# Kernel optimization log

Hardware: AMD Instinct MI355X
Metric: run time of the kernel (lower is better)

Reference implementation:

```python
import jax, jax.numpy as jnp
import numpy as np

B, W, K = 8, 128, 2048          # batch, window_size, n_features(=n_nodes)
D = 2 * W                        # embed_dim after the *2 in __init__ (embed_dim=None -> window_size)

def setup_inputs() -> dict:
    key = jax.random.key(0)
    k1, k2, k3, k4 = jax.random.split(key, 4)
    x = jax.random.normal(k1, (B, W, K), dtype=jnp.float32)
    # nn.Linear(2W -> D), stored as [in, out] so y = cat @ W_lin + b_lin
    lim = 1.0 / np.sqrt(2 * W)
    W_lin = jax.random.uniform(k2, (2 * W, D), dtype=jnp.float32, minval=-lim, maxval=lim)
    b_lin = jax.random.uniform(k3, (D,), dtype=jnp.float32, minval=-lim, maxval=lim)
    # a: xavier_uniform with gain=1.414 on shape (D, 1)
    a_lim = 1.414 * np.sqrt(6.0 / (D + 1))
    a = jax.random.uniform(k4, (D, 1), dtype=jnp.float32, minval=-a_lim, maxval=a_lim)
    bias = jnp.zeros((K, K), dtype=jnp.float32)
    return {"x": x, "W_lin": W_lin, "b_lin": b_lin, "a": a, "bias": bias}

def reference(x, W_lin, b_lin, a, bias):
    # x: [B, W, K] -> v: [B, K, W]
    v = jnp.transpose(x, (0, 2, 1))
    av = a[:, 0]                                  # [D]
    # lin(cat(v_i, v_j)) @ a == (v_i @ W1) @ a + (v_j @ W2) @ a + b_lin @ a
    # This avoids the O(K^2 * 2W) pairwise tensor; math identical to the original.
    W1, W2 = W_lin[:W], W_lin[W:]                 # each [W, D]
    u1 = jnp.einsum('bkw,wd,d->bk', v, W1, av)    # [B, K] source-side score
    u2 = jnp.einsum('bkw,wd,d->bk', v, W2, av)    # [B, K] target-side score
    e = u1[:, :, None] + u2[:, None, :] + jnp.dot(b_lin, av) + bias  # [B, K, K]
    attention = jax.nn.softmax(e, axis=2)         # dropout p=0.0 (eval) -> identity
    h = jax.nn.sigmoid(jnp.matmul(attention, v))  # [B, K, W]
    return jnp.transpose(h, (0, 2, 1))            # [B, W, K]
```

## Files before the change

kernel.cpp:

```cpp
#include <hip/hip_runtime.h>
#include <hip/hip_bf16.h>

#define B_ 8
#define W_ 128
#define K_ 2048
#define D_ 256
#define WX 144
#define NC 256

typedef __attribute__((ext_vector_type(8))) short bf16x8;
typedef __attribute__((ext_vector_type(4))) float f32x4;
typedef unsigned int u32;

static __device__ __forceinline__ short f2bf(float f) {
    unsigned int u = __float_as_uint(f);
    unsigned int r = (u + 0x7FFFu + ((u >> 16) & 1u)) >> 16;
    return (short)r;
}

__global__ void k_w2v(const float* __restrict__ W_lin, const float* __restrict__ a,
                      float* __restrict__ w2v) {
    int w = blockIdx.x, l = threadIdx.x;
    float4 rv = ((const float4*)(W_lin + (size_t)(W_ + w) * D_))[l];
    float4 av = ((const float4*)a)[l];
    float acc = rv.x * av.x + rv.y * av.y + rv.z * av.z + rv.w * av.w;
    for (int m = 1; m < 64; m <<= 1) acc += __shfl_xor(acc, m);
    if (l == 0) w2v[w] = acc;
}

__global__ __launch_bounds__(512) void k_pe(const float* __restrict__ x,
        const float* __restrict__ w2v, const float* __restrict__ bias,
        short* __restrict__ xbt, short* __restrict__ e2t) {
    __shared__ float sc[696];
    int tid = threadIdx.x;
    int wid = tid >> 6;
    int lane = tid & 63;

    if (blockIdx.x < 512) {
        if (tid < W_) sc[tid] = w2v[tid];
        __syncthreads();
        int q = tid & 31, cw = tid >> 5;
        int bk0 = blockIdx.x * 32;
        int b = bk0 >> 11;
        int k = (bk0 & (K_ - 1)) + q;
        const float* xp = x + ((size_t)b * W_ + cw * 8) * K_ + k;
        float xv[8];
        float acc = 0.f;
#pragma unroll
        for (int w = 0; w < 8; ++w) {
            xv[w] = xp[(size_t)w * K_];
            acc += xv[w] * sc[cw * 8 + w];
        }
        sc[128 + cw * 33 + q] = acc;
        __syncthreads();
        if (tid < 32) {
            float s = 0.f;
#pragma unroll
            for (int cc = 0; cc < 16; ++cc) s += sc[128 + cc * 33 + tid];
            sc[656 + tid] = __expf(s);
        }
        __syncthreads();
        float e1q = sc[656 + q];
        short* xo = xbt + (((size_t)b * NC + (k >> 3)) * WX + cw * 8) * 8 + (k & 7);
#pragma unroll
        for (int w = 0; w < 8; ++w) xo[w * 8] = f2bf(xv[w] * e1q);
        if (tid < 32) {
            int kk = (bk0 & (K_ - 1)) + tid;
            xbt[(((size_t)b * NC + (kk >> 3)) * WX + 128) * 8 + (kk & 7)] = f2bf(sc[656 + tid]);
        }
        if (tid >= 64 && tid < 124) {
            int id = tid - 64;
            int cl = id / 15, wz = 129 + id % 15;
            int c = ((bk0 & (K_ - 1)) >> 3) + cl;
            bf16x8 z = {0, 0, 0, 0, 0, 0, 0, 0};
            *(bf16x8*)(xbt + (((size_t)b * NC + c) * WX + wz) * 8) = z;
        }
    } else {
        int i0e = (int)(blockIdx.x - 512) * 4;
        int il = tid & 3, cg = tid >> 2;
        const float4* brow = (const float4*)(bias + (size_t)(i0e + il) * K_);
        float4 v0 = brow[cg * 4 + 0];
        float4 v1 = brow[cg * 4 + 1];
        float4 v2 = brow[cg * 4 + 2];
        float4 v3 = brow[cg * 4 + 3];
        float m = fmaxf(fmaxf(fmaxf(v0.x, v0.y), fmaxf(v0.z, v0.w)),
                        fmaxf(fmaxf(v1.x, v1.y), fmaxf(v1.z, v1.w)));
        m = fmaxf(m, fmaxf(fmaxf(fmaxf(v2.x, v2.y), fmaxf(v2.z, v2.w)),
                           fmaxf(fmaxf(v3.x, v3.y), fmaxf(v3.z, v3.w))));
#pragma unroll
        for (int mm = 4; mm < 64; mm <<= 1) m = fmaxf(m, __shfl_xor(m, mm));
        if (lane < 4) sc[wid * 4 + lane] = m;
        __syncthreads();
        float mb = sc[il];
#pragma unroll
        for (int w = 1; w < 8; ++w) mb = fmaxf(mb, sc[w * 4 + il]);
        bf16x8 o0, o1;
        o0[0] = f2bf(__expf(v0.x - mb)); o0[1] = f2bf(__expf(v0.y - mb));
        o0[2] = f2bf(__expf(v0.z - mb)); o0[3] = f2bf(__expf(v0.w - mb));
        o0[4] = f2bf(__expf(v1.x - mb)); o0[5] = f2bf(__expf(v1.y - mb));
        o0[6] = f2bf(__expf(v1.z - mb)); o0[7] = f2bf(__expf(v1.w - mb));
        o1[0] = f2bf(__expf(v2.x - mb)); o1[1] = f2bf(__expf(v2.y - mb));
        o1[2] = f2bf(__expf(v2.z - mb)); o1[3] = f2bf(__expf(v2.w - mb));
        o1[4] = f2bf(__expf(v3.x - mb)); o1[5] = f2bf(__expf(v3.y - mb));
        o1[6] = f2bf(__expf(v3.z - mb)); o1[7] = f2bf(__expf(v3.w - mb));
        int i = i0e + il;
        *(bf16x8*)(e2t + ((size_t)(cg * 2) * K_ + i) * 8)     = o0;
        *(bf16x8*)(e2t + ((size_t)(cg * 2 + 1) * K_ + i) * 8) = o1;
    }
}

#define MF(a_, b_, c_) __builtin_amdgcn_mfma_f32_16x16x32_bf16(a_, b_, c_, 0, 0, 0)

#define GLLDS(gsrc, ldst) __builtin_amdgcn_global_load_lds(                      \
    (const u32 __attribute__((address_space(1)))*)(const void*)(gsrc),           \
    (u32 __attribute__((address_space(3)))*)(void*)(ldst), 16, 0, 0)

#define WAITV(n_) asm volatile("s_waitcnt vmcnt(" #n_ ")" ::: "memory")
#define BARR __builtin_amdgcn_s_barrier()

__global__ __launch_bounds__(1024, 4) void k_gemm(const short* __restrict__ e2t,
        const short* __restrict__ xbt, float* __restrict__ out) {
    __shared__ __align__(16) char Bb[147456];
    int blk  = blockIdx.x;
    int b    = blk & 7;
    int i0   = (blk >> 3) * 64;
    int tid  = threadIdx.x;
    int wid  = tid >> 6;
    int lane = tid & 63;
    int il   = lane & 15;
    int kg   = lane >> 4;
    int m    = wid & 3;
    int jq   = wid >> 2;

    int i0r = i0 + m * 16;
    const short* eA = e2t + (((size_t)(jq * 64 + kg)) * K_ + i0r + il) * 8;
    size_t xbase = ((size_t)b * NC + jq * 64 + kg) * WX + il;
    char* jbuf = Bb + jq * 36864;

#define STG(s_) do {                                                             \
    const short* _g = xbt + (xbase + (size_t)(s_) * 4 * WX) * 8;                 \
    char* _d = jbuf + ((s_) & 3) * 9216;                                         \
    for (int f = m; f < 9; f += 4)                                               \
        GLLDS(_g + f * 128, _d + f * 1024);                                      \
} while (0)

#define FAix(sl_, s_) Ar##sl_ = *(const bf16x8*)(eA + (size_t)(s_) * 4 * K_ * 8)

    f32x4 q0{0,0,0,0}, q1{0,0,0,0}, q2{0,0,0,0}, q3{0,0,0,0}, q4{0,0,0,0},
          q5{0,0,0,0}, q6{0,0,0,0}, q7{0,0,0,0}, q8{0,0,0,0};

#define CONS(s_, sl_) do {                                                       \
    const char* _bp = jbuf + ((s_) & 3) * 9216;                                  \
    bf16x8 b0 = *(const bf16x8*)(_bp +    0 + lane * 16);                        \
    bf16x8 b1 = *(const bf16x8*)(_bp + 1024 + lane * 16);                        \
    bf16x8 b2 = *(const bf16x8*)(_bp + 2048 + lane * 16);                        \
    bf16x8 b3 = *(const bf16x8*)(_bp + 3072 + lane * 16);                        \
    bf16x8 b4 = *(const bf16x8*)(_bp + 4096 + lane * 16);                        \
    bf16x8 b5 = *(const bf16x8*)(_bp + 5120 + lane * 16);                        \
    bf16x8 b6 = *(const bf16x8*)(_bp + 6144 + lane * 16);                        \
    bf16x8 b7 = *(const bf16x8*)(_bp + 7168 + lane * 16);                        \
    bf16x8 b8 = *(const bf16x8*)(_bp + 8192 + lane * 16);                        \
    __builtin_amdgcn_s_setprio(1);                                               \
    q0 = MF(Ar##sl_, b0, q0); q1 = MF(Ar##sl_, b1, q1); q2 = MF(Ar##sl_, b2, q2);\
    q3 = MF(Ar##sl_, b3, q3); q4 = MF(Ar##sl_, b4, q4); q5 = MF(Ar##sl_, b5, q5);\
    q6 = MF(Ar##sl_, b6, q6); q7 = MF(Ar##sl_, b7, q7); q8 = MF(Ar##sl_, b8, q8);\
    __builtin_amdgcn_s_setprio(0);                                               \
} while (0)

#define STEP(s_, sl_, s2_, sl2_) do {                                            \
    FAix(sl2_, s2_); STG(s2_);                                                   \
    if (m == 0) WAITV(8); else WAITV(6);                                         \
    BARR;                                                                        \
    CONS(s_, sl_);                                                               \
} while (0)

    bf16x8 Ar0, Ar1, Ar2, Ar3;
    FAix(0, 0); STG(0);
    FAix(1, 1); STG(1);

    STEP(0, 0, 2, 2);   STEP(1, 1, 3, 3);
    STEP(2, 2, 4, 0);   STEP(3, 3, 5, 1);
    STEP(4, 0, 6, 2);   STEP(5, 1, 7, 3);
    STEP(6, 2, 8, 0);   STEP(7, 3, 9, 1);
    STEP(8, 0, 10, 2);  STEP(9, 1, 11, 3);
    STEP(10, 2, 12, 0); STEP(11, 3, 13, 1);
    STEP(12, 0, 14, 2); STEP(13, 1, 15, 3);
    if (m == 0) WAITV(4); else WAITV(3);
    BARR;
    CONS(14, 2);
    WAITV(0);
    BARR;
    CONS(15, 3);

    __syncthreads();

    f32x4* R = (f32x4*)Bb;
#define DUMPQ(base_) do {                                                        \
    f32x4* _r = R + ((base_) + m * 9) * 64 + lane;                               \
    _r[0*64] = q0; _r[1*64] = q1; _r[2*64] = q2; _r[3*64] = q3; _r[4*64] = q4;   \
    _r[5*64] = q5; _r[6*64] = q6; _r[7*64] = q7; _r[8*64] = q8; } while (0)
#define GATHQ(base_) do {                                                        \
    f32x4* _r = R + ((base_) + m * 9) * 64 + lane;                               \
    q0 += _r[0*64]; q1 += _r[1*64]; q2 += _r[2*64]; q3 += _r[3*64];              \
    q4 += _r[4*64]; q5 += _r[5*64]; q6 += _r[6*64]; q7 += _r[7*64];              \
    q8 += _r[8*64]; } while (0)

    if (jq >= 2) DUMPQ((jq - 2) * 36);
    __syncthreads();
    if (jq < 2) GATHQ(jq * 36);
    __syncthreads();
    if (jq == 1) DUMPQ(0);
    __syncthreads();
    if (jq == 0) {
        GATHQ(0);
        float linv0 = 1.f / __shfl(q8[0], kg * 16);
        float linv1 = 1.f / __shfl(q8[1], kg * 16);
        float linv2 = 1.f / __shfl(q8[2], kg * 16);
        float linv3 = 1.f / __shfl(q8[3], kg * 16);
        float* ob = out + (size_t)b * W_ * K_ + i0r + kg * 4;
#define STQ(n_, q_) do {                                                         \
        float4 o;                                                                \
        o.x = 1.f / (1.f + __expf(-q_[0] * linv0));                              \
        o.y = 1.f / (1.f + __expf(-q_[1] * linv1));                              \
        o.z = 1.f / (1.f + __expf(-q_[2] * linv2));                              \
        o.w = 1.f / (1.f + __expf(-q_[3] * linv3));                              \
        *(float4*)(ob + (size_t)((n_) * 16 + il) * K_) = o; } while (0)
        STQ(0, q0); STQ(1, q1); STQ(2, q2); STQ(3, q3);
        STQ(4, q4); STQ(5, q5); STQ(6, q6); STQ(7, q7);
#undef STQ
    }
}

extern "C" void kernel_launch(void* const* d_in, const int* in_sizes, int n_in,
                              void* d_out, int out_size, void* d_ws, size_t ws_size,
                              hipStream_t stream) {
    const float* x     = (const float*)d_in[0];
    const float* W_lin = (const float*)d_in[1];
    const float* a     = (const float*)d_in[3];
    const float* bias  = (const float*)d_in[4];
    float* out = (float*)d_out;

    float* w2v = (float*)d_ws;
    short* xbt = (short*)(w2v + 128);
    short* e2t = xbt + (size_t)B_ * NC * WX * 8;

    k_w2v <<<128, 64, 0, stream>>>(W_lin, a, w2v);
    k_pe  <<<1024, 512, 0, stream>>>(x, w2v, bias, xbt, e2t);
    k_gemm<<<256, 1024, 0, stream>>>(e2t, xbt, out);
}
```

Before: 34.32 us.

## Halve gemm block to 512 threads with two M-tiles per wave

Each wave in k_gemm now computes two 16-row output tiles (32 rows) instead of one. It reuses every LDS-loaded B fragment for two MFMAs, and the block shrinks from 16 to 8 waves. This cuts LDS read traffic per MFMA and the wave count, but doubles accumulator registers per wave and lowers occupancy and latency hiding. The wait counts, staging split and cross-wave reduction slots are adjusted to match.

Measured after the change: 36.62 us. 6.7% more time.

```diff
diff --git a/kernel.cpp b/kernel.cpp
--- a/kernel.cpp
+++ b/kernel.cpp
@@ -118,7 +118,7 @@
 #define WAITV(n_) asm volatile("s_waitcnt vmcnt(" #n_ ")" ::: "memory")
 #define BARR __builtin_amdgcn_s_barrier()
 
-__global__ __launch_bounds__(1024, 4) void k_gemm(const short* __restrict__ e2t,
+__global__ __launch_bounds__(512, 2) void k_gemm(const short* __restrict__ e2t,
         const short* __restrict__ xbt, float* __restrict__ out) {
     __shared__ __align__(16) char Bb[147456];
     int blk  = blockIdx.x;
@@ -129,10 +129,10 @@
     int lane = tid & 63;
     int il   = lane & 15;
     int kg   = lane >> 4;
-    int m    = wid & 3;
-    int jq   = wid >> 2;
-
-    int i0r = i0 + m * 16;
+    int mp   = wid & 1;
+    int jq   = wid >> 1;
+
+    int i0r = i0 + mp * 32;
     const short* eA = e2t + (((size_t)(jq * 64 + kg)) * K_ + i0r + il) * 8;
     size_t xbase = ((size_t)b * NC + jq * 64 + kg) * WX + il;
     char* jbuf = Bb + jq * 36864;
@@ -140,14 +140,20 @@
 #define STG(s_) do {                                                             \
     const short* _g = xbt + (xbase + (size_t)(s_) * 4 * WX) * 8;                 \
     char* _d = jbuf + ((s_) & 3) * 9216;                                         \
-    for (int f = m; f < 9; f += 4)                                               \
+    for (int f = mp; f < 9; f += 2)                                              \
         GLLDS(_g + f * 128, _d + f * 1024);                                      \
 } while (0)
 
-#define FAix(sl_, s_) Ar##sl_ = *(const bf16x8*)(eA + (size_t)(s_) * 4 * K_ * 8)
-
-    f32x4 q0{0,0,0,0}, q1{0,0,0,0}, q2{0,0,0,0}, q3{0,0,0,0}, q4{0,0,0,0},
-          q5{0,0,0,0}, q6{0,0,0,0}, q7{0,0,0,0}, q8{0,0,0,0};
+#define FAix(sl_, s_) do {                                                       \
+    const short* _e = eA + (size_t)(s_) * 4 * K_ * 8;                            \
+    ArA##sl_ = *(const bf16x8*)(_e);                                             \
+    ArB##sl_ = *(const bf16x8*)(_e + 128);                                       \
+} while (0)
+
+    f32x4 qa0{0,0,0,0}, qa1{0,0,0,0}, qa2{0,0,0,0}, qa3{0,0,0,0}, qa4{0,0,0,0},
+          qa5{0,0,0,0}, qa6{0,0,0,0}, qa7{0,0,0,0}, qa8{0,0,0,0};
+    f32x4 qb0{0,0,0,0}, qb1{0,0,0,0}, qb2{0,0,0,0}, qb3{0,0,0,0}, qb4{0,0,0,0},
+          qb5{0,0,0,0}, qb6{0,0,0,0}, qb7{0,0,0,0}, qb8{0,0,0,0};
 
 #define CONS(s_, sl_) do {                                                       \
     const char* _bp = jbuf + ((s_) & 3) * 9216;                                  \
@@ -161,20 +167,26 @@
     bf16x8 b7 = *(const bf16x8*)(_bp + 7168 + lane * 16);                        \
     bf16x8 b8 = *(const bf16x8*)(_bp + 8192 + lane * 16);                        \
     __builtin_amdgcn_s_setprio(1);                                               \
-    q0 = MF(Ar##sl_, b0, q0); q1 = MF(Ar##sl_, b1, q1); q2 = MF(Ar##sl_, b2, q2);\
-    q3 = MF(Ar##sl_, b3, q3); q4 = MF(Ar##sl_, b4, q4); q5 = MF(Ar##sl_, b5, q5);\
-    q6 = MF(Ar##sl_, b6, q6); q7 = MF(Ar##sl_, b7, q7); q8 = MF(Ar##sl_, b8, q8);\
+    qa0 = MF(ArA##sl_, b0, qa0); qb0 = MF(ArB##sl_, b0, qb0);                    \
+    qa1 = MF(ArA##sl_, b1, qa1); qb1 = MF(ArB##sl_, b1, qb1);                    \
+    qa2 = MF(ArA##sl_, b2, qa2); qb2 = MF(ArB##sl_, b2, qb2);                    \
+    qa3 = MF(ArA##sl_, b3, qa3); qb3 = MF(ArB##sl_, b3, qb3);                    \
+    qa4 = MF(ArA##sl_, b4, qa4); qb4 = MF(ArB##sl_, b4, qb4);                    \
+    qa5 = MF(ArA##sl_, b5, qa5); qb5 = MF(ArB##sl_, b5, qb5);                    \
+    qa6 = MF(ArA##sl_, b6, qa6); qb6 = MF(ArB##sl_, b6, qb6);                    \
+    qa7 = MF(ArA##sl_, b7, qa7); qb7 = MF(ArB##sl_, b7, qb7);                    \
+    qa8 = MF(ArA##sl_, b8, qa8); qb8 = MF(ArB##sl_, b8, qb8);                    \
     __builtin_amdgcn_s_setprio(0);                                               \
 } while (0)
 
 #define STEP(s_, sl_, s2_, sl2_) do {                                            \
     FAix(sl2_, s2_); STG(s2_);                                                   \
-    if (m == 0) WAITV(8); else WAITV(6);                                         \
+    if (mp == 0) WAITV(14); else WAITV(12);                                      \
     BARR;                                                                        \
     CONS(s_, sl_);                                                               \
 } while (0)
 
-    bf16x8 Ar0, Ar1, Ar2, Ar3;
+    bf16x8 ArA0, ArA1, ArA2, ArA3, ArB0, ArB1, ArB2, ArB3;
     FAix(0, 0); STG(0);
     FAix(1, 1); STG(1);
 
@@ -185,7 +197,7 @@
     STEP(8, 0, 10, 2);  STEP(9, 1, 11, 3);
     STEP(10, 2, 12, 0); STEP(11, 3, 13, 1);
     STEP(12, 0, 14, 2); STEP(13, 1, 15, 3);
-    if (m == 0) WAITV(4); else WAITV(3);
+    if (mp == 0) WAITV(7); else WAITV(6);
     BARR;
     CONS(14, 2);
     WAITV(0);
@@ -195,38 +207,53 @@
     __syncthreads();
 
     f32x4* R = (f32x4*)Bb;
-#define DUMPQ(base_) do {                                                        \
-    f32x4* _r = R + ((base_) + m * 9) * 64 + lane;                               \
-    _r[0*64] = q0; _r[1*64] = q1; _r[2*64] = q2; _r[3*64] = q3; _r[4*64] = q4;   \
-    _r[5*64] = q5; _r[6*64] = q6; _r[7*64] = q7; _r[8*64] = q8; } while (0)
-#define GATHQ(base_) do {                                                        \
-    f32x4* _r = R + ((base_) + m * 9) * 64 + lane;                               \
-    q0 += _r[0*64]; q1 += _r[1*64]; q2 += _r[2*64]; q3 += _r[3*64];              \
-    q4 += _r[4*64]; q5 += _r[5*64]; q6 += _r[6*64]; q7 += _r[7*64];              \
-    q8 += _r[8*64]; } while (0)
-
-    if (jq >= 2) DUMPQ((jq - 2) * 36);
-    __syncthreads();
-    if (jq < 2) GATHQ(jq * 36);
-    __syncthreads();
-    if (jq == 1) DUMPQ(0);
+#define DUMPQ(slot_) do {                                                        \
+    f32x4* _r = R + (size_t)(slot_) * 18 * 64 + lane;                            \
+    _r[0*64]=qa0; _r[1*64]=qa1; _r[2*64]=qa2; _r[3*64]=qa3; _r[4*64]=qa4;        \
+    _r[5*64]=qa5; _r[6*64]=qa6; _r[7*64]=qa7; _r[8*64]=qa8;                      \
+    _r[9*64]=qb0; _r[10*64]=qb1; _r[11*64]=qb2; _r[12*64]=qb3; _r[13*64]=qb4;    \
+    _r[14*64]=qb5; _r[15*64]=qb6; _r[16*64]=qb7; _r[17*64]=qb8; } while (0)
+#define GATHQ(slot_) do {                                                        \
+    f32x4* _r = R + (size_t)(slot_) * 18 * 64 + lane;                            \
+    qa0+=_r[0*64]; qa1+=_r[1*64]; qa2+=_r[2*64]; qa3+=_r[3*64]; qa4+=_r[4*64];   \
+    qa5+=_r[5*64]; qa6+=_r[6*64]; qa7+=_r[7*64]; qa8+=_r[8*64];                  \
+    qb0+=_r[9*64]; qb1+=_r[10*64]; qb2+=_r[11*64]; qb3+=_r[12*64];               \
+    qb4+=_r[13*64]; qb5+=_r[14*64]; qb6+=_r[15*64]; qb7+=_r[16*64];              \
+    qb8+=_r[17*64]; } while (0)
+
+    if (jq >= 2) DUMPQ((jq - 2) + 2 * mp);
+    __syncthreads();
+    if (jq < 2) GATHQ(jq + 2 * mp);
+    __syncthreads();
+    if (jq == 1) DUMPQ(mp);
     __syncthreads();
     if (jq == 0) {
-        GATHQ(0);
-        float linv0 = 1.f / __shfl(q8[0], kg * 16);
-        float linv1 = 1.f / __shfl(q8[1], kg * 16);
-        float linv2 = 1.f / __shfl(q8[2], kg * 16);
-        float linv3 = 1.f / __shfl(q8[3], kg * 16);
-        float* ob = out + (size_t)b * W_ * K_ + i0r + kg * 4;
-#define STQ(n_, q_) do {                                                         \
+        GATHQ(mp);
+        float lA0 = 1.f / __shfl(qa8[0], kg * 16);
+        float lA1 = 1.f / __shfl(qa8[1], kg * 16);
+        float lA2 = 1.f / __shfl(qa8[2], kg * 16);
+        float lA3 = 1.f / __shfl(qa8[3], kg * 16);
+        float lB0 = 1.f / __shfl(qb8[0], kg * 16);
+        float lB1 = 1.f / __shfl(qb8[1], kg * 16);
+        float lB2 = 1.f / __shfl(qb8[2], kg * 16);
+        float lB3 = 1.f / __shfl(qb8[3], kg * 16);
+        float* obA = out + (size_t)b * W_ * K_ + i0r + kg * 4;
+        float* obB = obA + 16;
+#define STQ(ob_, n_, q_, l0_, l1_, l2_, l3_) do {                                \
         float4 o;                                                                \
-        o.x = 1.f / (1.f + __expf(-q_[0] * linv0));                              \
-        o.y = 1.f / (1.f + __expf(-q_[1] * linv1));                              \
-        o.z = 1.f / (1.f + __expf(-q_[2] * linv2));                              \
-        o.w = 1.f / (1.f + __expf(-q_[3] * linv3));                              \
-        *(float4*)(ob + (size_t)((n_) * 16 + il) * K_) = o; } while (0)
-        STQ(0, q0); STQ(1, q1); STQ(2, q2); STQ(3, q3);
-        STQ(4, q4); STQ(5, q5); STQ(6, q6); STQ(7, q7);
+        o.x = 1.f / (1.f + __expf(-q_[0] * l0_));                                \
+        o.y = 1.f / (1.f + __expf(-q_[1] * l1_));                                \
+        o.z = 1.f / (1.f + __expf(-q_[2] * l2_));                                \
+        o.w = 1.f / (1.f + __expf(-q_[3] * l3_));                                \
+        *(float4*)(ob_ + (size_t)((n_) * 16 + il) * K_) = o; } while (0)
+        STQ(obA, 0, qa0, lA0, lA1, lA2, lA3); STQ(obB, 0, qb0, lB0, lB1, lB2, lB3);
+        STQ(obA, 1, qa1, lA0, lA1, lA2, lA3); STQ(obB, 1, qb1, lB0, lB1, lB2, lB3);
+        STQ(obA, 2, qa2, lA0, lA1, lA2, lA3); STQ(obB, 2, qb2, lB0, lB1, lB2, lB3);
+        STQ(obA, 3, qa3, lA0, lA1, lA2, lA3); STQ(obB, 3, qb3, lB0, lB1, lB2, lB3);
+        STQ(obA, 4, qa4, lA0, lA1, lA2, lA3); STQ(obB, 4, qb4, lB0, lB1, lB2, lB3);
+        STQ(obA, 5, qa5, lA0, lA1, lA2, lA3); STQ(obB, 5, qb5, lB0, lB1, lB2, lB3);
+        STQ(obA, 6, qa6, lA0, lA1, lA2, lA3); STQ(obB, 6, qb6, lB0, lB1, lB2, lB3);
+        STQ(obA, 7, qa7, lA0, lA1, lA2, lA3); STQ(obB, 7, qb7, lB0, lB1, lB2, lB3);
 #undef STQ
     }
 }
@@ -246,5 +273,5 @@
 
     k_w2v <<<128, 64, 0, stream>>>(W_lin, a, w2v);
     k_pe  <<<1024, 512, 0, stream>>>(x, w2v, bias, xbt, e2t);
-    k_gemm<<<256, 1024, 0, stream>>>(e2t, xbt, out);
-}
+    k_gemm<<<256, 512, 0, stream>>>(e2t, xbt, out);
+}
```
